# Performance work log

Hardware: AMD Instinct MI355X
Metric: run time of the kernel (lower is better)

The kernel has to match this reference:

```python
import jax, jax.numpy as jnp
import numpy as np

ALPHA = 0.2      # LeakyReLU negative slope
EPS = 1e-5       # LayerNorm eps (torch default)
NEG = -9e15      # mask value from the original module

N, IN_F, OUT_F = 8192, 256, 64


def setup_inputs() -> dict:
    key = jax.random.key(0)
    k1, k2, k3, k4, k5 = jax.random.split(key, 5)
    inp = {
        "input": jax.random.normal(k1, (N, IN_F), dtype=jnp.float32),
        "adj": jax.random.randint(k2, (N, N), 0, 2, dtype=jnp.int32),
        "W": jax.random.normal(k3, (IN_F, OUT_F), dtype=jnp.float32) * (1.414 * (6.0 / (IN_F + OUT_F)) ** 0.5),
        "a1": jax.random.normal(k4, (OUT_F,), dtype=jnp.float32) * 0.2,
        "a2": jax.random.normal(k5, (OUT_F,), dtype=jnp.float32) * 0.2,
        "gamma": jnp.ones((OUT_F,), dtype=jnp.float32),
        "beta": jnp.zeros((OUT_F,), dtype=jnp.float32),
    }
    return inp


def reference(input, adj, W, a1, a2, gamma, beta):
    h = input @ W                                    # [N, F]
    # a^T [Wh_i || Wh_j] = (Wh_i @ a1) + (Wh_j @ a2)  (exact decomposition)
    f = h @ a1                                       # [N]
    g = h @ a2                                       # [N]
    e = jax.nn.leaky_relu(f[:, None] + g[None, :], ALPHA)   # [N, N]
    e = jnp.where(adj > 0, e, jnp.float32(NEG))
    attention = jax.nn.softmax(e, axis=1)            # [N, N]  (dropout p=0 -> identity)
    h_prime = attention @ h                          # [N, F]
    # LayerNorm over feature dim
    mu = jnp.mean(h_prime, axis=-1, keepdims=True)
    var = jnp.mean((h_prime - mu) ** 2, axis=-1, keepdims=True)
    h_norm = (h_prime - mu) * jax.lax.rsqrt(var + EPS) * gamma + beta
    return jax.nn.elu(h_norm)                        # concat=True -> ELU
```

## Files before the change

kernel.cpp:

```cpp
#include <hip/hip_runtime.h>
#include <math.h>

#define N      8192
#define IN_F   256
#define OUT_F  64
#define ALPHA  0.2f
#define LN_EPS 1e-5f
#define KVB    256
#define NCH    (N / KVB)

typedef __attribute__((ext_vector_type(8))) short bf16x8;
typedef __attribute__((ext_vector_type(4))) short s16x4;
typedef __attribute__((ext_vector_type(4))) float f32x4;
typedef __attribute__((ext_vector_type(4))) int   i32x4;

#define BAR() do { asm volatile("s_waitcnt lgkmcnt(0)" ::: "memory"); \
                   __builtin_amdgcn_s_barrier(); } while (0)

__device__ __forceinline__ float wave_sum(float v) {
#pragma unroll
    for (int off = 32; off >= 1; off >>= 1) v += __shfl_xor(v, off, 64);
    return v;
}

__device__ __forceinline__ short f2bf(float x) {
    union { float f; unsigned u; } v; v.f = x;
    unsigned r = v.u + 0x7FFF + ((v.u >> 16) & 1);
    return (short)(r >> 16);
}
__device__ __forceinline__ float bf2f(short b) {
    union { unsigned u; float f; } v; v.u = ((unsigned)(unsigned short)b) << 16;
    return v.f;
}

__global__ __launch_bounds__(256) void gat_phaseA(
    const float* __restrict__ input, const float* __restrict__ W,
    const float* __restrict__ a1, const float* __restrict__ a2,
    unsigned short* __restrict__ hB, float* __restrict__ fv, float* __restrict__ gv)
{
    const int lane = threadIdx.x & 63;
    const int wid  = threadIdx.x >> 6;
    const int blockRow0 = blockIdx.x * 32;
    const int i0 = blockRow0 + wid * 8;

    float hacc[8];
#pragma unroll
    for (int r = 0; r < 8; r++) hacc[r] = 0.f;

    for (int k = 0; k < IN_F; k += 4) {
        const float w0 = W[(k + 0) * OUT_F + lane];
        const float w1 = W[(k + 1) * OUT_F + lane];
        const float w2 = W[(k + 2) * OUT_F + lane];
        const float w3 = W[(k + 3) * OUT_F + lane];
#pragma unroll
        for (int r = 0; r < 8; r++) {
            const float4 iv = *(const float4*)&input[(size_t)(i0 + r) * IN_F + k];
            hacc[r] = fmaf(iv.x, w0, hacc[r]);
            hacc[r] = fmaf(iv.y, w1, hacc[r]);
            hacc[r] = fmaf(iv.z, w2, hacc[r]);
            hacc[r] = fmaf(iv.w, w3, hacc[r]);
        }
    }

    const float a1v = a1[lane];
    const float a2v = a2[lane];

    __shared__ float hsm[32][65];
#pragma unroll
    for (int r = 0; r < 8; r++) {
        hsm[wid * 8 + r][lane] = hacc[r];
        const float fr = wave_sum(hacc[r] * a1v);
        const float gr = wave_sum(hacc[r] * a2v);
        if (lane == 0) { fv[i0 + r] = fr; gv[i0 + r] = gr; }
    }
    __syncthreads();

    const int f  = threadIdx.x >> 2;
    const int cp = threadIdx.x & 3;
    union { unsigned short s[8]; int4 v; } pk;
#pragma unroll
    for (int c = 0; c < 8; c++) pk.s[c] = (unsigned short)f2bf(hsm[cp * 8 + c][f]);
    *(int4*)&hB[(size_t)((blockRow0 >> 3) + cp) * 512 + f * 8] = pk.v;
}

__global__ __launch_bounds__(256) void gat_attn(
    const int* __restrict__ adj, const unsigned short* __restrict__ hB,
    const float* __restrict__ fv, const float* __restrict__ gv,
    const float* __restrict__ gamma, const float* __restrict__ beta,
    float* __restrict__ out)
{
    __shared__ short wls[16][264];
    __shared__ float lnbuf[16][68];
    __shared__ float denbuf[16];

    const int tid  = threadIdx.x;
    const int lane = tid & 63;
    const int wid  = tid >> 6;
    const int n16  = lane & 15;
    const int g4   = lane >> 4;
    const int rowBase = blockIdx.x * 16;
    const int rbase   = rowBase + wid * 4;

    float frow[4];
#pragma unroll
    for (int rr = 0; rr < 4; ++rr) frow[rr] = fv[rbase + rr];

    f32x4 acc = {0.f, 0.f, 0.f, 0.f};
    float dp[4] = {0.f, 0.f, 0.f, 0.f};

    i32x4  adjA[4], adjB[4];
    float4 gA, gB;

#define PREFETCH(GC, ADJ, G) do {                                              \
    const size_t jp = (size_t)(GC) * KVB;                                      \
    _Pragma("unroll")                                                          \
    for (int rr = 0; rr < 4; ++rr)                                             \
        ADJ[rr] = __builtin_nontemporal_load(                                  \
            (const i32x4*)(adj + (size_t)(rbase + rr) * N + jp + lane * 4));   \
    G = *(const float4*)(gv + jp + lane * 4);                                  \
} while (0)

#define STEP(C, ADJ, G, NADJ, NG) do {                                         \
        \
    bf16x8 breg[8];                                                            \
    {                                                                          \
        const unsigned short* hb = hB + (size_t)((C) * 32 + g4) * 512          \
                                   + wid * 128 + n16 * 8;                      \
        _Pragma("unroll")                                                      \
        for (int ks = 0; ks < 8; ++ks)                                         \
            breg[ks] = *(const bf16x8*)(hb + (size_t)ks * 2048);               \
    }                                                                          \
    const int pc = ((C) + 1 < NCH) ? (C) + 1 : (C);                            \
    PREFETCH(pc, NADJ, NG);                                                    \
    BAR();                \
    _Pragma("unroll")                                                          \
    for (int rr = 0; rr < 4; ++rr) {                                           \
        s16x4 pk;                                                              \
        _Pragma("unroll")                                                      \
        for (int e = 0; e < 4; ++e) {                                          \
            float t = frow[rr] + ((const float*)&G)[e];                        \
            t = fmaxf(t, ALPHA * t);                           \
            const float w = (((const int*)&ADJ[rr])[e] > 0) ? __expf(t) : 0.f; \
            const short wb = f2bf(w);                                          \
            dp[rr] += bf2f(wb);                                                \
            pk[e] = wb;                                                        \
        }                                                                      \
        *(s16x4*)&wls[wid * 4 + rr][lane * 4] = pk;                            \
    }                                                                          \
    BAR();                                      \
    _Pragma("unroll")                                                          \
    for (int ks = 0; ks < 8; ++ks) {                                           \
        bf16x8 a = *(const bf16x8*)&wls[n16][ks * 32 + g4 * 8];                \
        acc = __builtin_amdgcn_mfma_f32_16x16x32_bf16(a, breg[ks], acc, 0, 0, 0); \
    }                                                                          \
} while (0)

    PREFETCH(0, adjA, gA);
    for (int c = 0; c < NCH; c += 2) {
        STEP(c,     adjA, gA, adjB, gB);
        STEP(c + 1, adjB, gB, adjA, gA);
    }
#undef STEP
#undef PREFETCH

#pragma unroll
    for (int rr = 0; rr < 4; ++rr) {
        const float dr = wave_sum(dp[rr]);
        if (lane == 0) denbuf[wid * 4 + rr] = dr;
    }

#pragma unroll
    for (int r = 0; r < 4; ++r) lnbuf[g4 * 4 + r][wid * 16 + n16] = acc[r];
    __syncthreads();

    const int r = tid >> 4;
    const int q = tid & 15;
    const float den = denbuf[r];
    float4 v = *(const float4*)&lnbuf[r][q * 4];
    const float inv = 1.0f / den;
    v.x *= inv; v.y *= inv; v.z *= inv; v.w *= inv;

    float sm = v.x + v.y + v.z + v.w;
#pragma unroll
    for (int o = 1; o < 16; o <<= 1) sm += __shfl_xor(sm, o, 64);
    const float mu = sm * (1.0f / 64.0f);

    const float dx = v.x - mu, dy = v.y - mu, dz = v.z - mu, dw = v.w - mu;
    float ss = dx * dx + dy * dy + dz * dz + dw * dw;
#pragma unroll
    for (int o = 1; o < 16; o <<= 1) ss += __shfl_xor(ss, o, 64);
    const float rs = rsqrtf(ss * (1.0f / 64.0f) + LN_EPS);

    const float4 gm = *(const float4*)&gamma[q * 4];
    const float4 bt = *(const float4*)&beta[q * 4];
    float y0 = dx * rs * gm.x + bt.x;
    float y1 = dy * rs * gm.y + bt.y;
    float y2 = dz * rs * gm.z + bt.z;
    float y3 = dw * rs * gm.w + bt.w;
    y0 = (y0 > 0.f) ? y0 : expm1f(y0);
    y1 = (y1 > 0.f) ? y1 : expm1f(y1);
    y2 = (y2 > 0.f) ? y2 : expm1f(y2);
    y3 = (y3 > 0.f) ? y3 : expm1f(y3);
    *(float4*)&out[(size_t)(rowBase + r) * OUT_F + q * 4] = make_float4(y0, y1, y2, y3);
}

extern "C" void kernel_launch(void* const* d_in, const int* in_sizes, int n_in,
                              void* d_out, int out_size, void* d_ws, size_t ws_size,
                              hipStream_t stream)
{
    const float* input = (const float*)d_in[0];
    const int*   adj   = (const int*)d_in[1];
    const float* W     = (const float*)d_in[2];
    const float* a1    = (const float*)d_in[3];
    const float* a2    = (const float*)d_in[4];
    const float* gamma = (const float*)d_in[5];
    const float* beta  = (const float*)d_in[6];
    float* out = (float*)d_out;

    unsigned short* hB = (unsigned short*)d_ws;
    float* fv = (float*)(hB + (size_t)OUT_F * N);
    float* gv = fv + N;

    gat_phaseA<<<N / 32, 256, 0, stream>>>(input, W, a1, a2, hB, fv, gv);
    gat_attn<<<N / 16, 256, 0, stream>>>(adj, hB, fv, gv, gamma, beta, out);
}
```

Baseline: 89.43 us.

## Compress adjacency into a bitmask in a separate pass before attention

```diff
diff --git a/kernel.cpp b/kernel.cpp
--- a/kernel.cpp
+++ b/kernel.cpp
@@ -8,6 +8,7 @@
 #define LN_EPS 1e-5f
 #define KVB    256
 #define NCH    (N / KVB)
+#define NW     (N / 32)
 
 typedef __attribute__((ext_vector_type(8))) short bf16x8;
 typedef __attribute__((ext_vector_type(4))) short s16x4;
@@ -83,8 +84,25 @@
     *(int4*)&hB[(size_t)((blockRow0 >> 3) + cp) * 512 + f * 8] = pk.v;
 }
 
+__global__ __launch_bounds__(256) void gat_compress(
+    const int* __restrict__ adj, unsigned* __restrict__ bm)
+{
+    const size_t gtid = (size_t)blockIdx.x * 256 + threadIdx.x;
+    const int lane = threadIdx.x & 63;
+    const size_t nthr = (size_t)2048 * 256;
+#pragma unroll 4
+    for (size_t i = gtid; i < (size_t)N * N; i += nthr) {
+        const int v = __builtin_nontemporal_load(adj + i);
+        const unsigned long long m = __ballot(v > 0);
+        if (lane < 2)
+            bm[((i - lane) >> 5) + lane] = (unsigned)(m >> (lane * 32));
+    }
+}
+
+template <int USEBM>
 __global__ __launch_bounds__(256) void gat_attn(
-    const int* __restrict__ adj, const unsigned short* __restrict__ hB,
+    const int* __restrict__ adj, const unsigned* __restrict__ bm,
+    const unsigned short* __restrict__ hB,
     const float* __restrict__ fv, const float* __restrict__ gv,
     const float* __restrict__ gamma, const float* __restrict__ beta,
     float* __restrict__ out)
@@ -108,20 +126,27 @@
     f32x4 acc = {0.f, 0.f, 0.f, 0.f};
     float dp[4] = {0.f, 0.f, 0.f, 0.f};
 
-    i32x4  adjA[4], adjB[4];
-    float4 gA, gB;
-
-#define PREFETCH(GC, ADJ, G) do {                                              \
+    i32x4    adjA[4], adjB[4];
+    unsigned bwA[4],  bwB[4];
+    float4   gA, gB;
+
+#define PREFETCH(GC, ADJ, BW, G) do {                                          \
     const size_t jp = (size_t)(GC) * KVB;                                      \
-    _Pragma("unroll")                                                          \
-    for (int rr = 0; rr < 4; ++rr)                                             \
-        ADJ[rr] = __builtin_nontemporal_load(                                  \
-            (const i32x4*)(adj + (size_t)(rbase + rr) * N + jp + lane * 4));   \
+    if (USEBM) {                                                               \
+        _Pragma("unroll")                                                      \
+        for (int rr = 0; rr < 4; ++rr)                                         \
+            BW[rr] = bm[(size_t)(rbase + rr) * NW + (jp >> 5) + (lane >> 3)];  \
+    } else {                                                                   \
+        _Pragma("unroll")                                                      \
+        for (int rr = 0; rr < 4; ++rr)                                         \
+            ADJ[rr] = __builtin_nontemporal_load(                              \
+                (const i32x4*)(adj + (size_t)(rbase + rr) * N + jp + lane * 4)); \
+    }                                                                          \
     G = *(const float4*)(gv + jp + lane * 4);                                  \
 } while (0)
 
-#define STEP(C, ADJ, G, NADJ, NG) do {                                         \
-        \
+#define STEP(C, ADJ, BW, G, NADJ, NBW, NG) do {                                \
+            \
     bf16x8 breg[8];                                                            \
     {                                                                          \
         const unsigned short* hb = hB + (size_t)((C) * 32 + g4) * 512          \
@@ -131,7 +156,7 @@
             breg[ks] = *(const bf16x8*)(hb + (size_t)ks * 2048);               \
     }                                                                          \
     const int pc = ((C) + 1 < NCH) ? (C) + 1 : (C);                            \
-    PREFETCH(pc, NADJ, NG);                                                    \
+    PREFETCH(pc, NADJ, NBW, NG);                                               \
     BAR();                \
     _Pragma("unroll")                                                          \
     for (int rr = 0; rr < 4; ++rr) {                                           \
@@ -140,7 +165,10 @@
         for (int e = 0; e < 4; ++e) {                                          \
             float t = frow[rr] + ((const float*)&G)[e];                        \
             t = fmaxf(t, ALPHA * t);                           \
-            const float w = (((const int*)&ADJ[rr])[e] > 0) ? __expf(t) : 0.f; \
+            int av;                                                            \
+            if (USEBM) av = (int)((BW[rr] >> ((lane & 7) * 4 + e)) & 1u);      \
+            else       av = (((const int*)&ADJ[rr])[e] > 0) ? 1 : 0;           \
+            const float w = av ? __expf(t) : 0.0f;                             \
             const short wb = f2bf(w);                                          \
             dp[rr] += bf2f(wb);                                                \
             pk[e] = wb;                                                        \
@@ -155,10 +183,10 @@
     }                                                                          \
 } while (0)
 
-    PREFETCH(0, adjA, gA);
+    PREFETCH(0, adjA, bwA, gA);
     for (int c = 0; c < NCH; c += 2) {
-        STEP(c,     adjA, gA, adjB, gB);
-        STEP(c + 1, adjB, gB, adjA, gA);
+        STEP(c,     adjA, bwA, gA, adjB, bwB, gB);
+        STEP(c + 1, adjB, bwB, gB, adjA, bwA, gA);
     }
 #undef STEP
 #undef PREFETCH
@@ -218,9 +246,16 @@
     float* out = (float*)d_out;
 
     unsigned short* hB = (unsigned short*)d_ws;
-    float* fv = (float*)(hB + (size_t)OUT_F * N);
+    float* fv = (float*)((char*)d_ws + 1048576);
     float* gv = fv + N;
+    unsigned* bm = (unsigned*)((char*)d_ws + 1048576 + 65536);
+    const size_t needBig = 1048576 + 65536 + (size_t)N * NW * 4;
 
     gat_phaseA<<<N / 32, 256, 0, stream>>>(input, W, a1, a2, hB, fv, gv);
-    gat_attn<<<N / 16, 256, 0, stream>>>(adj, hB, fv, gv, gamma, beta, out);
-}
+    if (ws_size >= needBig) {
+        gat_compress<<<2048, 256, 0, stream>>>(adj, bm);
+        gat_attn<1><<<N / 16, 256, 0, stream>>>(adj, bm, hB, fv, gv, gamma, beta, out);
+    } else {
+        gat_attn<0><<<N / 16, 256, 0, stream>>>(adj, bm, hB, fv, gv, gamma, beta, out);
+    }
+}
```

New measurement: 148.9 us. +66.5%, slower.
